# Kernel tuning notes

Hardware: AMD Instinct MI355X
Metric: run time of the kernel (lower is better)

Reference implementation:

```python
import jax, jax.numpy as jnp
import numpy as np

N_NODES, N_EDGES = 50000, 25000
MAX_ARITY, MAX_DEG = 6, 8
NFEAT, NHID, NEMB, NHEADS = 128, 64, 128, 4
BATCH = 4096
ALPHA = 0.2
NEG = -1e9


def _attn_layer(hn_in, he_in, edge_list, node_list, Wn, We, a1, a2, concat):
    # hn_in [N,fin_n], he_in [E,fin_e]; edge_list [E,A] 1-based (0=pad); node_list [N,D] 1-based (0=pad)
    hn = hn_in @ Wn                      # [N,d]
    he = he_in @ We                      # [E,d]
    # --- stage 1: node -> edge attention ---
    emask = edge_list > 0                # [E,A]
    eidx = jnp.where(emask, edge_list - 1, 0)
    nd = hn[eidx]                        # [E,A,d]
    he_b = jnp.broadcast_to(he[:, None, :], nd.shape)
    s1 = jax.nn.leaky_relu(jnp.concatenate([he_b, nd], -1) @ a1, ALPHA)  # [E,A]
    att1 = jax.nn.softmax(jnp.where(emask, s1, NEG), axis=-1)
    edge_out = jnp.einsum('ea,ead->ed', att1, nd)  # [E,d]
    # --- stage 2: edge -> node attention ---
    nmask = node_list > 0                # [N,D]
    nidx = jnp.where(nmask, node_list - 1, 0)
    ed = edge_out[nidx]                  # [N,D,d]
    hn_b = jnp.broadcast_to(hn[:, None, :], ed.shape)
    s2 = jax.nn.leaky_relu(jnp.concatenate([hn_b, ed], -1) @ a2, ALPHA)  # [N,D]
    att2 = jax.nn.softmax(jnp.where(nmask, s2, NEG), axis=-1)
    node_out = jnp.einsum('nd,nde->ne', att2, ed)  # [N,d]
    if concat:
        node_out, edge_out = jax.nn.elu(node_out), jax.nn.elu(edge_out)
    return node_out, edge_out


def _forward(batch_inputs, edge_list, node_list, node_embs, edge_embs,
             Wn, We, a1, a2, Wn_o, We_o, a1_o, a2_o):
    # multi-head layers (vmap over head-stacked params)
    heads = jax.vmap(_attn_layer, in_axes=(None, None, None, None, 0, 0, 0, 0, None))
    hn, he = heads(node_embs, edge_embs, edge_list, node_list, Wn, We, a1, a2, True)
    H, N, d = hn.shape
    out_n = jnp.transpose(hn, (1, 0, 2)).reshape(N, H * d)          # concat heads
    out_e = jnp.transpose(he, (1, 0, 2)).reshape(he.shape[1], H * d)
    # dropout is identity in eval mode
    out_n, out_e = _attn_layer(out_n, out_e, edge_list, node_list, Wn_o, We_o, a1_o, a2_o, False)
    out_n, out_e = jax.nn.elu(out_n), jax.nn.elu(out_e)
    # --- build batch_outputs ---
    B, A1 = batch_inputs.shape
    nemb = out_e.shape[1]
    row0 = out_e[batch_inputs[:, 0] - 1]                            # [B,nemb] (col0 always >0)
    nids = batch_inputs[:, 1:] - 1
    nids = jnp.where(nids < 0, nids + out_n.shape[0], nids)         # torch-style negative wrap
    gathered = out_n[nids]                                          # [B,A1-1,nemb]
    last_nz = jnp.max(jnp.where(batch_inputs != 0, jnp.arange(A1)[None, :], -1), axis=1)  # right-1
    fill = (jnp.arange(1, A1)[None, :] <= last_nz[:, None])[:, :, None]
    rest = jnp.where(fill, gathered, jnp.ones((), gathered.dtype))
    return jnp.concatenate([row0[:, None, :], rest], axis=1)        # [B,A1,nemb]


def setup_inputs() -> dict:
    key = jax.random.key(0)
    ks = jax.random.split(key, 12)
    f32 = jnp.float32
    node_embs = jax.random.normal(ks[0], (N_NODES, NFEAT), f32) * 0.02
    edge_embs = jax.random.normal(ks[1], (N_EDGES, NFEAT), f32) * 0.02
    # ragged incidence with 0-padding (1-based ids)
    el = jax.random.randint(ks[2], (N_EDGES, MAX_ARITY), 1, N_NODES + 1)
    earity = jax.random.randint(ks[3], (N_EDGES, 1), 2, MAX_ARITY + 1)
    edge_list = jnp.where(jnp.arange(MAX_ARITY)[None, :] < earity, el, 0)
    nl = jax.random.randint(ks[4], (N_NODES, MAX_DEG), 1, N_EDGES + 1)
    ndeg = jax.random.randint(ks[5], (N_NODES, 1), 1, MAX_DEG + 1)
    node_list = jnp.where(jnp.arange(MAX_DEG)[None, :] < ndeg, nl, 0)
    # batch: col0 = edge id, cols 1.. = node ids, right-padded with 0
    bi_e = jax.random.randint(ks[6], (BATCH, 1), 1, N_EDGES + 1)
    bi_n = jax.random.randint(ks[7], (BATCH, MAX_ARITY), 1, N_NODES + 1)
    barity = jax.random.randint(ks[8], (BATCH, 1), 2, MAX_ARITY + 1)
    bi_n = jnp.where(jnp.arange(MAX_ARITY)[None, :] < barity, bi_n, 0)
    batch_inputs = jnp.concatenate([bi_e, bi_n], axis=1)
    def glorot(k, shape):
        lim = np.sqrt(6.0 / (shape[-2] + shape[-1]))
        return jax.random.uniform(k, shape, f32, -lim, lim)
    return {
        'batch_inputs': batch_inputs, 'edge_list': edge_list, 'node_list': node_list,
        'node_embs': node_embs, 'edge_embs': edge_embs,
        'Wn': glorot(ks[9], (NHEADS, NFEAT, NHID)),
        'We': glorot(ks[10], (NHEADS, NFEAT, NHID)),
        'a1': jax.random.normal(ks[11], (NHEADS, 2 * NHID), f32) * 0.1,
        'a2': jax.random.normal(jax.random.fold_in(key, 20), (NHEADS, 2 * NHID), f32) * 0.1,
        'Wn_o': glorot(jax.random.fold_in(key, 21), (NHID * NHEADS, NEMB)),
        'We_o': glorot(jax.random.fold_in(key, 22), (NHID * NHEADS, NEMB)),
        'a1_o': jax.random.normal(jax.random.fold_in(key, 23), (2 * NEMB,), f32) * 0.1,
        'a2_o': jax.random.normal(jax.random.fold_in(key, 24), (2 * NEMB,), f32) * 0.1,
    }


def reference(batch_inputs, edge_list, node_list, node_embs, edge_embs,
              Wn, We, a1, a2, Wn_o, We_o, a1_o, a2_o):
    return _forward(batch_inputs, edge_list, node_list, node_embs, edge_embs,
                    Wn, We, a1, a2, Wn_o, We_o, a1_o, a2_o)
```

## Files before the change

### kernel.cpp

```cpp
#include <hip/hip_runtime.h>
#include <math.h>

#define N_NODES 50000
#define N_EDGES 25000
#define MAX_ARITY 6
#define MAX_DEG 8
#define NFEAT 128
#define NHID 64
#define NEMB 128
#define NHEADS 4
#define BATCH 4096

#define MT_N 3128

typedef __bf16 bf16x8 __attribute__((ext_vector_type(8)));
typedef __bf16 bf16x4 __attribute__((ext_vector_type(4)));
typedef float f32x4 __attribute__((ext_vector_type(4)));
typedef float f32x2 __attribute__((ext_vector_type(2)));

__device__ __forceinline__ float wave_sum(float v) {
#pragma unroll
    for (int off = 1; off < 64; off <<= 1) v += __shfl_xor(v, off);
    return v;
}
__device__ __forceinline__ float group32_sum(float v) {
#pragma unroll
    for (int off = 1; off < 32; off <<= 1) v += __shfl_xor(v, off);
    return v;
}
__device__ __forceinline__ float group16_sum(float v) {
#pragma unroll
    for (int off = 1; off < 16; off <<= 1) v += __shfl_xor(v, off);
    return v;
}
__device__ __forceinline__ float group8_sum(float v) {
#pragma unroll
    for (int off = 1; off < 8; off <<= 1) v += __shfl_xor(v, off);
    return v;
}
__device__ __forceinline__ float lrelu(float x) { return x >= 0.f ? x : 0.2f * x; }
__device__ __forceinline__ float eluf(float x) { return x > 0.f ? x : expm1f(x); }

__device__ __forceinline__ int2 pack_fp8x8(const float* v) {
    int w0 = __builtin_amdgcn_cvt_pk_fp8_f32(v[0], v[1], 0, 0);
    w0 = __builtin_amdgcn_cvt_pk_fp8_f32(v[2], v[3], w0, 1);
    int w1 = __builtin_amdgcn_cvt_pk_fp8_f32(v[4], v[5], 0, 0);
    w1 = __builtin_amdgcn_cvt_pk_fp8_f32(v[6], v[7], w1, 1);
    int2 o;
    o.x = w0;
    o.y = w1;
    return o;
}
__device__ __forceinline__ void unpack_fp8x8(int2 w, float* v) {
    f32x2 a = __builtin_amdgcn_cvt_pk_f32_fp8(w.x, false);
    f32x2 b = __builtin_amdgcn_cvt_pk_f32_fp8(w.x, true);
    f32x2 c = __builtin_amdgcn_cvt_pk_f32_fp8(w.y, false);
    f32x2 d = __builtin_amdgcn_cvt_pk_f32_fp8(w.y, true);
    v[0] = a[0]; v[1] = a[1]; v[2] = b[0]; v[3] = b[1];
    v[4] = c[0]; v[5] = c[1]; v[6] = d[0]; v[7] = d[1];
}
__device__ __forceinline__ unsigned char fp8_of(float x) {
    return (unsigned char)(__builtin_amdgcn_cvt_pk_fp8_f32(x, x, 0, 0) & 0xff);
}

#define PREP_BCONV1_BLKS 16
#define PREP_BCONV2_BLKS 16
#define PREP_WVEC1_BLKS 2
#define PREP_WVEC2_BLKS 1
#define PREP_C1_BLKS 6250
#define PREP_TOTAL_BLKS (PREP_BCONV1_BLKS + PREP_BCONV2_BLKS + \
                         PREP_WVEC1_BLKS + PREP_WVEC2_BLKS + PREP_C1_BLKS)

__global__ __launch_bounds__(256) void prep_kernel(
    const float* __restrict__ edge_embs, const float* __restrict__ Wn,
    const float* __restrict__ We, const float* __restrict__ a1, const float* __restrict__ Wn_o,
    const float* __restrict__ We_o, const float* __restrict__ a1_o, __bf16* __restrict__ B1n,
    __bf16* __restrict__ B2n, float* __restrict__ wc1, float* __restrict__ wc2,
    float* __restrict__ c1) {
    int blk = blockIdx.x;
    if (blk < PREP_BCONV1_BLKS) {
        int t = blk * 256 + threadIdx.x;
        int lane = t & 63;
        int nt = (t >> 6) & 15;
        int kt = t >> 10;
        int k0 = kt * 32 + (lane >> 4) * 8;
        int h = nt >> 2;
        int nl = (nt & 3) * 16 + (lane & 15);
        bf16x8 o;
#pragma unroll
        for (int j = 0; j < 8; ++j) o[j] = (__bf16)Wn[(h * NFEAT + k0 + j) * NHID + nl];
        reinterpret_cast<bf16x8*>(B1n)[t] = o;
        return;
    }
    blk -= PREP_BCONV1_BLKS;
    if (blk < PREP_BCONV2_BLKS) {
        int t = blk * 256 + threadIdx.x;
        int lane = t & 63;
        int nt = (t >> 6) & 7;
        int kt = t >> 9;
        int k0 = kt * 32 + (lane >> 4) * 8;
        int n = nt * 16 + (lane & 15);
        bf16x8 o;
#pragma unroll
        for (int j = 0; j < 8; ++j) o[j] = (__bf16)Wn_o[(size_t)(k0 + j) * 128 + n];
        reinterpret_cast<bf16x8*>(B2n)[t] = o;
        return;
    }
    blk -= PREP_BCONV2_BLKS;
    if (blk < PREP_WVEC1_BLKS) {
        int t = blk * 256 + threadIdx.x;
        int h = t >> 7, k = t & 127;
        float s = 0.f;
        for (int j = 0; j < 64; ++j) s += We[(h * NFEAT + k) * NHID + j] * a1[h * 128 + j];
        wc1[t] = s;
        return;
    }
    blk -= PREP_WVEC1_BLKS;
    if (blk < PREP_WVEC2_BLKS) {
        int t = threadIdx.x;
        float s = 0.f;
        for (int j = 0; j < 128; ++j) s += We_o[(size_t)t * 128 + j] * a1_o[j];
        wc2[t] = s;
        return;
    }
    blk -= PREP_WVEC2_BLKS;
    {
        int r = blk * 4 + (threadIdx.x >> 6);
        int lane = threadIdx.x & 63;
        if (r >= N_EDGES) return;
        float x0 = edge_embs[(size_t)r * 128 + lane];
        float x1 = edge_embs[(size_t)r * 128 + 64 + lane];
#pragma unroll
        for (int h = 0; h < 4; ++h) {
            float s = wave_sum(x0 * wc1[h * 128 + lane] + x1 * wc1[h * 128 + 64 + lane]);
            if (lane == 0) c1[r * 4 + h] = s;
        }
    }
}

__global__ __launch_bounds__(256) void mgemm1_kernel(
    const float* __restrict__ Af32, const __bf16* __restrict__ B,
    unsigned char* __restrict__ C, const float* __restrict__ a1v,
    const float* __restrict__ a2v, float* __restrict__ d1, float* __restrict__ g1v) {
    const int w = threadIdx.x >> 6, l = threadIdx.x & 63;
    const int mtb = blockIdx.y * 8 + w * 2;
    const int nbf = blockIdx.x * 4;
    const int lr = l & 15, lk = (l >> 4) * 8;
    f32x4 acc[2][4];
#pragma unroll
    for (int i = 0; i < 2; ++i)
#pragma unroll
        for (int j = 0; j < 4; ++j) acc[i][j] = (f32x4){0.f, 0.f, 0.f, 0.f};
    const bf16x8* Bp = reinterpret_cast<const bf16x8*>(B) + l;
#pragma unroll
    for (int kt = 0; kt < 4; ++kt) {
        bf16x8 a[2];
#pragma unroll
        for (int mi = 0; mi < 2; ++mi) {
            int row = (mtb + mi) * 16 + lr;
            int ks = kt * 32 + lk;
            float v[8];
            if (row < N_NODES) {
                float4 p0 = *reinterpret_cast<const float4*>(Af32 + (size_t)row * 128 + ks);
                float4 p1 = *reinterpret_cast<const float4*>(Af32 + (size_t)row * 128 + ks + 4);
                v[0] = p0.x; v[1] = p0.y; v[2] = p0.z; v[3] = p0.w;
                v[4] = p1.x; v[5] = p1.y; v[6] = p1.z; v[7] = p1.w;
            } else {
#pragma unroll
                for (int j = 0; j < 8; ++j) v[j] = 0.f;
            }
#pragma unroll
            for (int j = 0; j < 8; ++j) a[mi][j] = (__bf16)v[j];
        }
#pragma unroll
        for (int nj = 0; nj < 4; ++nj) {
            bf16x8 b = Bp[((size_t)kt * 16 + nbf + nj) * 64];
#pragma unroll
            for (int mi = 0; mi < 2; ++mi)
                acc[mi][nj] = __builtin_amdgcn_mfma_f32_16x16x32_bf16(a[mi], b, acc[mi][nj], 0, 0, 0);
        }
    }
    const int rq = (l >> 4) * 4;
    const int cl = l & 15;
    const int h = nbf >> 2;
    float va[4], vb[4];
#pragma unroll
    for (int nj = 0; nj < 4; ++nj) {
        int col = ((nbf + nj) & 3) * 16 + cl;
        va[nj] = a1v[h * 128 + 64 + col];
        vb[nj] = a2v[h * 128 + col];
    }
#pragma unroll
    for (int mi = 0; mi < 2; ++mi) {
#pragma unroll
        for (int q = 0; q < 4; ++q) {
            int m = (mtb + mi) * 16 + rq + q;
            float pA = 0.f, pB = 0.f;
#pragma unroll
            for (int nj = 0; nj < 4; ++nj) {
                pA += acc[mi][nj][q] * va[nj];
                pB += acc[mi][nj][q] * vb[nj];
            }
            if (m < N_NODES) {
#pragma unroll
                for (int nj = 0; nj < 4; ++nj)
                    C[(size_t)m * 256 + (nbf + nj) * 16 + cl] = fp8_of(acc[mi][nj][q]);
            }
            pA = group16_sum(pA);
            pB = group16_sum(pB);
            if (cl == 0 && m < N_NODES) {
                d1[m * 4 + h] = pA;
                g1v[m * 4 + h] = pB;
            }
        }
    }
}

__global__ __launch_bounds__(256) void attn64e_kernel(
    const int* __restrict__ nbr, const unsigned char* __restrict__ feat,
    const float* __restrict__ sdot, const float* __restrict__ ndot,
    const float* __restrict__ a2v, const float* __restrict__ wc2,
    unsigned char* __restrict__ eo1, float* __restrict__ f1, float* __restrict__ c2, int rows) {
    const int lane = threadIdx.x & 63;
    const int half = lane >> 5, lp = lane & 31;
    const int r = (blockIdx.x * 4 + (threadIdx.x >> 6)) * 2 + half;
    if (r >= rows) return;
    const int h = lp >> 3;
    int id[MAX_ARITY];
    bool val[MAX_ARITY];
#pragma unroll
    for (int a = 0; a < MAX_ARITY; ++a) {
        int v = nbr[r * MAX_ARITY + a];
        val[a] = v > 0;
        id[a] = val[a] ? (v - 1) : 0;
    }
    int2 f8[MAX_ARITY];
    float nd[MAX_ARITY];
#pragma unroll
    for (int a = 0; a < MAX_ARITY; ++a) {
        f8[a] = *reinterpret_cast<const int2*>(feat + (size_t)id[a] * 256 + lp * 8);
        nd[a] = ndot[(size_t)id[a] * 4 + h];
    }
    const float c = sdot[r * 4 + h];
    float wgt[MAX_ARITY];
    float smax = -1e30f;
#pragma unroll
    for (int a = 0; a < MAX_ARITY; ++a) {
        float s = val[a] ? lrelu(c + nd[a]) : -3e30f;
        wgt[a] = s;
        if (val[a]) smax = fmaxf(smax, s);
    }
    float denom = 0.f;
#pragma unroll
    for (int a = 0; a < MAX_ARITY; ++a) {
        float ex = val[a] ? expf(wgt[a] - smax) : 0.f;
        wgt[a] = ex;
        denom += ex;
    }
    float inv = 1.f / denom;
    float acc[8] = {0.f, 0.f, 0.f, 0.f, 0.f, 0.f, 0.f, 0.f};
#pragma unroll
    for (int a = 0; a < MAX_ARITY; ++a) {
        float fv[8];
        unpack_fp8x8(f8[a], fv);
#pragma unroll
        for (int j = 0; j < 8; ++j) acc[j] = fmaf(wgt[a], fv[j], acc[j]);
    }
#pragma unroll
    for (int j = 0; j < 8; ++j) acc[j] *= inv;
    *reinterpret_cast<int2*>(eo1 + (size_t)r * 256 + lp * 8) = pack_fp8x8(acc);
    float p = 0.f;
#pragma unroll
    for (int j = 0; j < 8; ++j) p += acc[j] * a2v[h * 128 + 64 + (lp & 7) * 8 + j];
    p = group8_sum(p);
    if ((lp & 7) == 0) f1[r * 4 + h] = p;
    float p2 = 0.f;
#pragma unroll
    for (int j = 0; j < 8; ++j) p2 += eluf(acc[j]) * wc2[lp * 8 + j];
    p2 = group32_sum(p2);
    if (lp == 0) c2[r] = p2;
}

#define LDSW 260

__global__ __launch_bounds__(256) void fuse2_kernel(
    const int* __restrict__ nbr, const unsigned char* __restrict__ feat,
    const float* __restrict__ sdot, const float* __restrict__ ndot,
    const __bf16* __restrict__ B, __bf16* __restrict__ hn2, const float* __restrict__ a1o,
    const float* __restrict__ a2o, float* __restrict__ d2, float* __restrict__ g2v) {
    __shared__ __bf16 Alds[64 * LDSW];
    const int w = threadIdx.x >> 6, lane = threadIdx.x & 63;
    const int half = lane >> 5, lp = lane & 31;
    const int h = lp >> 3;
#pragma unroll
    for (int p = 0; p < 8; ++p) {
        const int rl = w * 16 + p * 2 + half;
        const int r = blockIdx.x * 64 + rl;
        __bf16* dptr = &Alds[rl * LDSW + lp * 8];
        if (r >= N_NODES) {
            bf16x8 z;
#pragma unroll
            for (int j = 0; j < 8; ++j) z[j] = (__bf16)0.f;
            *reinterpret_cast<bf16x8*>(dptr) = z;
            continue;
        }
        int id[MAX_DEG];
        bool val[MAX_DEG];
#pragma unroll
        for (int a = 0; a < MAX_DEG; ++a) {
            int v = nbr[r * MAX_DEG + a];
            val[a] = v > 0;
            id[a] = val[a] ? (v - 1) : 0;
        }
        int2 f8[MAX_DEG];
        float nd[MAX_DEG];
#pragma unroll
        for (int a = 0; a < MAX_DEG; ++a) {
            f8[a] = *reinterpret_cast<const int2*>(feat + (size_t)id[a] * 256 + lp * 8);
            nd[a] = ndot[(size_t)id[a] * 4 + h];
        }
        const float c = sdot[r * 4 + h];
        float wgt[MAX_DEG];
        float smax = -1e30f;
#pragma unroll
        for (int a = 0; a < MAX_DEG; ++a) {
            float s = val[a] ? lrelu(c + nd[a]) : -3e30f;
            wgt[a] = s;
            if (val[a]) smax = fmaxf(smax, s);
        }
        float denom = 0.f;
#pragma unroll
        for (int a = 0; a < MAX_DEG; ++a) {
            float ex = val[a] ? expf(wgt[a] - smax) : 0.f;
            wgt[a] = ex;
            denom += ex;
        }
        float inv = 1.f / denom;
        float acc[8] = {0.f, 0.f, 0.f, 0.f, 0.f, 0.f, 0.f, 0.f};
#pragma unroll
        for (int a = 0; a < MAX_DEG; ++a) {
            float fv[8];
            unpack_fp8x8(f8[a], fv);
#pragma unroll
            for (int j = 0; j < 8; ++j) acc[j] = fmaf(wgt[a], fv[j], acc[j]);
        }
        bf16x8 o;
#pragma unroll
        for (int j = 0; j < 8; ++j) o[j] = (__bf16)eluf(acc[j] * inv);
        *reinterpret_cast<bf16x8*>(dptr) = o;
    }
    __syncthreads();
    const int lr = lane & 15, lkq = lane >> 4;
    f32x4 acc[8];
#pragma unroll
    for (int j = 0; j < 8; ++j) acc[j] = (f32x4){0.f, 0.f, 0.f, 0.f};
    const bf16x8* Bp = reinterpret_cast<const bf16x8*>(B) + lane;
#pragma unroll
    for (int kt = 0; kt < 8; ++kt) {
        bf16x8 a = *reinterpret_cast<const bf16x8*>(
            &Alds[(w * 16 + lr) * LDSW + kt * 32 + lkq * 8]);
#pragma unroll
        for (int nj = 0; nj < 8; ++nj) {
            bf16x8 b = Bp[((size_t)kt * 8 + nj) * 64];
            acc[nj] = __builtin_amdgcn_mfma_f32_16x16x32_bf16(a, b, acc[nj], 0, 0, 0);
        }
    }
    const int rq = lkq * 4;
    const int cl = lane & 15;
    const int gm0 = blockIdx.x * 64 + w * 16 + rq;
    float va[8], vb[8];
#pragma unroll
    for (int nj = 0; nj < 8; ++nj) {
        va[nj] = a1o[128 + nj * 16 + cl];
        vb[nj] = a2o[nj * 16 + cl];
    }
#pragma unroll
    for (int q = 0; q < 4; ++q) {
        int m = gm0 + q;
        float pA = 0.f, pB = 0.f;
#pragma unroll
        for (int nj = 0; nj < 8; ++nj) {
            pA += acc[nj][q] * va[nj];
            pB += acc[nj][q] * vb[nj];
        }
        if (m < N_NODES) {
#pragma unroll
            for (int nj = 0; nj < 8; ++nj)
                hn2[(size_t)m * 128 + nj * 16 + cl] = (__bf16)acc[nj][q];
        }
        pA = group16_sum(pA);
        pB = group16_sum(pB);
        if (cl == 0 && m < N_NODES) {
            d2[m] = pA;
            g2v[m] = pB;
        }
    }
}

template <int NNBR, bool DOT>
__global__ __launch_bounds__(256) void attn128_kernel(const int* __restrict__ nbr,
                                                      const __bf16* __restrict__ feat,
                                                      const float* __restrict__ sdot,
                                                      const float* __restrict__ ndot,
                                                      const float* __restrict__ fvec,
                                                      __bf16* __restrict__ outF,
                                                      float* __restrict__ outDot, int rows) {
    const int lane = threadIdx.x & 63;
    const int qt = lane >> 4, lq = lane & 15;
    const int r = (blockIdx.x * 4 + (threadIdx.x >> 6)) * 4 + qt;
    if (r >= rows) return;
    int id[NNBR];
    bool val[NNBR];
#pragma unroll
    for (int a = 0; a < NNBR; ++a) {
        int v = nbr[r * NNBR + a];
        val[a] = v > 0;
        id[a] = val[a] ? (v - 1) : 0;
    }
    bf16x8 f8[NNBR];
    float nd[NNBR];
#pragma unroll
    for (int a = 0; a < NNBR; ++a) {
        f8[a] = *reinterpret_cast<const bf16x8*>(feat + (size_t)id[a] * 128 + lq * 8);
        nd[a] = ndot[id[a]];
    }
    const float c = sdot[r];
    float wgt[NNBR];
    float smax = -1e30f;
#pragma unroll
    for (int a = 0; a < NNBR; ++a) {
        float s = val[a] ? lrelu(c + nd[a]) : -3e30f;
        wgt[a] = s;
        if (val[a]) smax = fmaxf(smax, s);
    }
    float denom = 0.f;
#pragma unroll
    for (int a = 0; a < NNBR; ++a) {
        float ex = val[a] ? expf(wgt[a] - smax) : 0.f;
        wgt[a] = ex;
        denom += ex;
    }
    float inv = 1.f / denom;
    float acc[8] = {0.f, 0.f, 0.f, 0.f, 0.f, 0.f, 0.f, 0.f};
#pragma unroll
    for (int a = 0; a < NNBR; ++a)
#pragma unroll
        for (int j = 0; j < 8; ++j) acc[j] = fmaf(wgt[a], (float)f8[a][j], acc[j]);
    bf16x8 o;
#pragma unroll
    for (int j = 0; j < 8; ++j) {
        acc[j] *= inv;
        o[j] = (__bf16)acc[j];
    }
    *reinterpret_cast<bf16x8*>(outF + (size_t)r * 128 + lq * 8) = o;
    if (DOT) {
        float p = 0.f;
#pragma unroll
        for (int j = 0; j < 8; ++j) p += acc[j] * fvec[128 + lq * 8 + j];
        p = group16_sum(p);
        if (lq == 0) outDot[r] = p;
    }
}

__global__ __launch_bounds__(256) void batch_kernel(const int* __restrict__ bi,
                                                    const __bf16* __restrict__ eo2,
                                                    const __bf16* __restrict__ no2,
                                                    float* __restrict__ out) {
    const int lane = threadIdx.x & 63;
    const int half = lane >> 5, lp = lane & 31;
    const int gw = (blockIdx.x * 4 + (threadIdx.x >> 6)) * 2 + half;
    if (gw >= BATCH * 7) return;
    int b = gw / 7, s = gw % 7;
    int last_nz = -1;
#pragma unroll
    for (int j = 0; j < 7; ++j)
        if (bi[b * 7 + j] != 0) last_nz = j;
    float4 v;
    if (s == 0) {
        int e = bi[b * 7] - 1;
        bf16x4 t = *reinterpret_cast<const bf16x4*>(eo2 + (size_t)e * 128 + lp * 4);
        v = make_float4(eluf((float)t[0]), eluf((float)t[1]), eluf((float)t[2]),
                        eluf((float)t[3]));
    } else if (s <= last_nz) {
        int nid = bi[b * 7 + s] - 1;
        if (nid < 0) nid += N_NODES;
        bf16x4 t = *reinterpret_cast<const bf16x4*>(no2 + (size_t)nid * 128 + lp * 4);
        v = make_float4(eluf((float)t[0]), eluf((float)t[1]), eluf((float)t[2]),
                        eluf((float)t[3]));
    } else {
        v = make_float4(1.f, 1.f, 1.f, 1.f);
    }
    *reinterpret_cast<float4*>(out + (size_t)b * 896 + s * 128 + lp * 4) = v;
}

extern "C" void kernel_launch(void* const* d_in, const int* in_sizes, int n_in,
                              void* d_out, int out_size, void* d_ws, size_t ws_size,
                              hipStream_t stream) {
    const int* batch_inputs = (const int*)d_in[0];
    const int* edge_list = (const int*)d_in[1];
    const int* node_list = (const int*)d_in[2];
    const float* node_embs = (const float*)d_in[3];
    const float* edge_embs = (const float*)d_in[4];
    const float* Wn = (const float*)d_in[5];
    const float* We = (const float*)d_in[6];
    const float* a1 = (const float*)d_in[7];
    const float* a2 = (const float*)d_in[8];
    const float* Wn_o = (const float*)d_in[9];
    const float* We_o = (const float*)d_in[10];
    const float* a1_o = (const float*)d_in[11];
    const float* a2_o = (const float*)d_in[12];
    float* out = (float*)d_out;
    char* ws = (char*)d_ws;

    __bf16* B1n = (__bf16*)(ws);
    __bf16* B2n = (__bf16*)(ws + 65536);
    float* wc1 = (float*)(ws + 131072);
    float* wc2 = (float*)(ws + 133120);
    float* c1 = (float*)(ws + 134144);
    float* d1 = (float*)(ws + 534144);
    float* g1v = (float*)(ws + 1334144);
    float* f1 = (float*)(ws + 2134144);
    float* c2 = (float*)(ws + 2534144);
    float* d2 = (float*)(ws + 2634144);
    float* g2v = (float*)(ws + 2834144);
    float* f2 = (float*)(ws + 3034144);
    unsigned char* hn1 = (unsigned char*)(ws + 3134144);
    __bf16* hn2 = (__bf16*)(ws + 15934144);
    unsigned char* eo1 = (unsigned char*)(ws + 28734144);
    __bf16* eo2 = (__bf16*)(ws + 35134144);
    __bf16* no2 = (__bf16*)(ws + 41534144);

    prep_kernel<<<PREP_TOTAL_BLKS, 256, 0, stream>>>(edge_embs, Wn, We, a1, Wn_o, We_o, a1_o,
                                                     B1n, B2n, wc1, wc2, c1);

    {
        dim3 g(4, MT_N / 8);
        mgemm1_kernel<<<g, 256, 0, stream>>>(node_embs, B1n, hn1, a1, a2, d1, g1v);
    }
    attn64e_kernel<<<(N_EDGES / 2 + 3) / 4, 256, 0, stream>>>(edge_list, hn1, c1, d1, a2, wc2,
                                                              eo1, f1, c2, N_EDGES);
    fuse2_kernel<<<MT_N / 4, 256, 0, stream>>>(node_list, eo1, g1v, f1, B2n, hn2, a1_o, a2_o,
                                               d2, g2v);
    attn128_kernel<MAX_ARITY, true><<<(N_EDGES / 4 + 3) / 4, 256, 0, stream>>>(
        edge_list, hn2, c2, d2, a2_o, eo2, f2, N_EDGES);
    attn128_kernel<MAX_DEG, false><<<(N_NODES / 4 + 3) / 4, 256, 0, stream>>>(
        node_list, eo2, g2v, f2, nullptr, no2, nullptr, N_NODES);
    batch_kernel<<<(BATCH * 7 / 2 + 3) / 4, 256, 0, stream>>>(batch_inputs, eo2, no2, out);
}
```

Baseline: 218.5 us.

## Compute final node attention only for batch-referenced nodes; unfuse layer-2 GEMM

```diff
diff --git a/kernel.cpp b/kernel.cpp
--- a/kernel.cpp
+++ b/kernel.cpp
@@ -216,6 +216,57 @@
     }
 }
 
+__global__ __launch_bounds__(256) void mgemm2_kernel(
+    const __bf16* __restrict__ A, const __bf16* __restrict__ B, __bf16* __restrict__ C,
+    const float* __restrict__ a1o, const float* __restrict__ a2o, float* __restrict__ d2,
+    float* __restrict__ g2v) {
+    const int w = threadIdx.x >> 6, l = threadIdx.x & 63;
+    const int mtb = blockIdx.y * 4 + w;
+    f32x4 acc[8];
+#pragma unroll
+    for (int j = 0; j < 8; ++j) acc[j] = (f32x4){0.f, 0.f, 0.f, 0.f};
+    const bf16x8* Ap = reinterpret_cast<const bf16x8*>(A) + (size_t)mtb * 8 * 64 + l;
+    const bf16x8* Bp = reinterpret_cast<const bf16x8*>(B) + l;
+#pragma unroll
+    for (int kt = 0; kt < 8; ++kt) {
+        bf16x8 a = Ap[(size_t)kt * 64];
+#pragma unroll
+        for (int nj = 0; nj < 8; ++nj) {
+            bf16x8 b = Bp[((size_t)kt * 8 + nj) * 64];
+            acc[nj] = __builtin_amdgcn_mfma_f32_16x16x32_bf16(a, b, acc[nj], 0, 0, 0);
+        }
+    }
+    const int rq = (l >> 4) * 4;
+    const int cl = l & 15;
+    float va[8], vb[8];
+#pragma unroll
+    for (int nj = 0; nj < 8; ++nj) {
+        va[nj] = a1o[128 + nj * 16 + cl];
+        vb[nj] = a2o[nj * 16 + cl];
+    }
+#pragma unroll
+    for (int q = 0; q < 4; ++q) {
+        int m = mtb * 16 + rq + q;
+        float pA = 0.f, pB = 0.f;
+#pragma unroll
+        for (int nj = 0; nj < 8; ++nj) {
+            pA += acc[nj][q] * va[nj];
+            pB += acc[nj][q] * vb[nj];
+        }
+        if (m < N_NODES) {
+#pragma unroll
+            for (int nj = 0; nj < 8; ++nj)
+                C[(size_t)m * 128 + nj * 16 + cl] = (__bf16)acc[nj][q];
+        }
+        pA = group16_sum(pA);
+        pB = group16_sum(pB);
+        if (cl == 0 && m < N_NODES) {
+            d2[m] = pA;
+            g2v[m] = pB;
+        }
+    }
+}
+
 __global__ __launch_bounds__(256) void attn64e_kernel(
     const int* __restrict__ nbr, const unsigned char* __restrict__ feat,
     const float* __restrict__ sdot, const float* __restrict__ ndot,
@@ -281,161 +332,109 @@
     if (lp == 0) c2[r] = p2;
 }
 
-#define LDSW 260
-
-__global__ __launch_bounds__(256) void fuse2_kernel(
-    const int* __restrict__ nbr, const unsigned char* __restrict__ feat,
-    const float* __restrict__ sdot, const float* __restrict__ ndot,
-    const __bf16* __restrict__ B, __bf16* __restrict__ hn2, const float* __restrict__ a1o,
-    const float* __restrict__ a2o, float* __restrict__ d2, float* __restrict__ g2v) {
-    __shared__ __bf16 Alds[64 * LDSW];
-    const int w = threadIdx.x >> 6, lane = threadIdx.x & 63;
-    const int half = lane >> 5, lp = lane & 31;
-    const int h = lp >> 3;
-#pragma unroll
-    for (int p = 0; p < 8; ++p) {
-        const int rl = w * 16 + p * 2 + half;
-        const int r = blockIdx.x * 64 + rl;
-        __bf16* dptr = &Alds[rl * LDSW + lp * 8];
-        if (r >= N_NODES) {
-            bf16x8 z;
-#pragma unroll
-            for (int j = 0; j < 8; ++j) z[j] = (__bf16)0.f;
-            *reinterpret_cast<bf16x8*>(dptr) = z;
-            continue;
-        }
-        int id[MAX_DEG];
-        bool val[MAX_DEG];
-#pragma unroll
-        for (int a = 0; a < MAX_DEG; ++a) {
-            int v = nbr[r * MAX_DEG + a];
-            val[a] = v > 0;
-            id[a] = val[a] ? (v - 1) : 0;
-        }
-        int2 f8[MAX_DEG];
-        float nd[MAX_DEG];
-#pragma unroll
-        for (int a = 0; a < MAX_DEG; ++a) {
-            f8[a] = *reinterpret_cast<const int2*>(feat + (size_t)id[a] * 256 + lp * 8);
-            nd[a] = ndot[(size_t)id[a] * 4 + h];
-        }
-        const float c = sdot[r * 4 + h];
-        float wgt[MAX_DEG];
-        float smax = -1e30f;
-#pragma unroll
-        for (int a = 0; a < MAX_DEG; ++a) {
-            float s = val[a] ? lrelu(c + nd[a]) : -3e30f;
-            wgt[a] = s;
-            if (val[a]) smax = fmaxf(smax, s);
-        }
-        float denom = 0.f;
-#pragma unroll
-        for (int a = 0; a < MAX_DEG; ++a) {
-            float ex = val[a] ? expf(wgt[a] - smax) : 0.f;
-            wgt[a] = ex;
-            denom += ex;
-        }
-        float inv = 1.f / denom;
-        float acc[8] = {0.f, 0.f, 0.f, 0.f, 0.f, 0.f, 0.f, 0.f};
-#pragma unroll
-        for (int a = 0; a < MAX_DEG; ++a) {
-            float fv[8];
-            unpack_fp8x8(f8[a], fv);
-#pragma unroll
-            for (int j = 0; j < 8; ++j) acc[j] = fmaf(wgt[a], fv[j], acc[j]);
-        }
-        bf16x8 o;
-#pragma unroll
-        for (int j = 0; j < 8; ++j) o[j] = (__bf16)eluf(acc[j] * inv);
-        *reinterpret_cast<bf16x8*>(dptr) = o;
-    }
-    __syncthreads();
-    const int lr = lane & 15, lkq = lane >> 4;
-    f32x4 acc[8];
-#pragma unroll
-    for (int j = 0; j < 8; ++j) acc[j] = (f32x4){0.f, 0.f, 0.f, 0.f};
-    const bf16x8* Bp = reinterpret_cast<const bf16x8*>(B) + lane;
-#pragma unroll
-    for (int kt = 0; kt < 8; ++kt) {
-        bf16x8 a = *reinterpret_cast<const bf16x8*>(
-            &Alds[(w * 16 + lr) * LDSW + kt * 32 + lkq * 8]);
-#pragma unroll
-        for (int nj = 0; nj < 8; ++nj) {
-            bf16x8 b = Bp[((size_t)kt * 8 + nj) * 64];
-            acc[nj] = __builtin_amdgcn_mfma_f32_16x16x32_bf16(a, b, acc[nj], 0, 0, 0);
-        }
-    }
-    const int rq = lkq * 4;
-    const int cl = lane & 15;
-    const int gm0 = blockIdx.x * 64 + w * 16 + rq;
-    float va[8], vb[8];
-#pragma unroll
-    for (int nj = 0; nj < 8; ++nj) {
-        va[nj] = a1o[128 + nj * 16 + cl];
-        vb[nj] = a2o[nj * 16 + cl];
-    }
-#pragma unroll
-    for (int q = 0; q < 4; ++q) {
-        int m = gm0 + q;
-        float pA = 0.f, pB = 0.f;
-#pragma unroll
-        for (int nj = 0; nj < 8; ++nj) {
-            pA += acc[nj][q] * va[nj];
-            pB += acc[nj][q] * vb[nj];
-        }
-        if (m < N_NODES) {
-#pragma unroll
-            for (int nj = 0; nj < 8; ++nj)
-                hn2[(size_t)m * 128 + nj * 16 + cl] = (__bf16)acc[nj][q];
-        }
-        pA = group16_sum(pA);
-        pB = group16_sum(pB);
-        if (cl == 0 && m < N_NODES) {
-            d2[m] = pA;
-            g2v[m] = pB;
-        }
-    }
-}
-
-template <int NNBR, bool DOT>
-__global__ __launch_bounds__(256) void attn128_kernel(const int* __restrict__ nbr,
-                                                      const __bf16* __restrict__ feat,
+__global__ __launch_bounds__(256) void attn64n_kernel(const int* __restrict__ nbr,
+                                                      const unsigned char* __restrict__ feat,
                                                       const float* __restrict__ sdot,
                                                       const float* __restrict__ ndot,
-                                                      const float* __restrict__ fvec,
-                                                      __bf16* __restrict__ outF,
-                                                      float* __restrict__ outDot, int rows) {
+                                                      __bf16* __restrict__ Afrag, int rows,
+                                                      int rowsPad) {
+    const int lane = threadIdx.x & 63;
+    const int half = lane >> 5, lp = lane & 31;
+    const int r = (blockIdx.x * 4 + (threadIdx.x >> 6)) * 2 + half;
+    if (r >= rowsPad) return;
+    const int rr = r & 15, mt = r >> 4;
+    const int kt = lp >> 2, g = lp & 3;
+    __bf16* dptr = Afrag + ((((size_t)mt * 8 + kt) * 64 + g * 16 + rr) << 3);
+    if (r >= rows) {
+        bf16x8 z;
+#pragma unroll
+        for (int j = 0; j < 8; ++j) z[j] = (__bf16)0.f;
+        *reinterpret_cast<bf16x8*>(dptr) = z;
+        return;
+    }
+    const int h = lp >> 3;
+    int id[MAX_DEG];
+    bool val[MAX_DEG];
+#pragma unroll
+    for (int a = 0; a < MAX_DEG; ++a) {
+        int v = nbr[r * MAX_DEG + a];
+        val[a] = v > 0;
+        id[a] = val[a] ? (v - 1) : 0;
+    }
+    int2 f8[MAX_DEG];
+    float nd[MAX_DEG];
+#pragma unroll
+    for (int a = 0; a < MAX_DEG; ++a) {
+        f8[a] = *reinterpret_cast<const int2*>(feat + (size_t)id[a] * 256 + lp * 8);
+        nd[a] = ndot[(size_t)id[a] * 4 + h];
+    }
+    const float c = sdot[r * 4 + h];
+    float wgt[MAX_DEG];
+    float smax = -1e30f;
+#pragma unroll
+    for (int a = 0; a < MAX_DEG; ++a) {
+        float s = val[a] ? lrelu(c + nd[a]) : -3e30f;
+        wgt[a] = s;
+        if (val[a]) smax = fmaxf(smax, s);
+    }
+    float denom = 0.f;
+#pragma unroll
+    for (int a = 0; a < MAX_DEG; ++a) {
+        float ex = val[a] ? expf(wgt[a] - smax) : 0.f;
+        wgt[a] = ex;
+        denom += ex;
+    }
+    float inv = 1.f / denom;
+    float acc[8] = {0.f, 0.f, 0.f, 0.f, 0.f, 0.f, 0.f, 0.f};
+#pragma unroll
+    for (int a = 0; a < MAX_DEG; ++a) {
+        float fv[8];
+        unpack_fp8x8(f8[a], fv);
+#pragma unroll
+        for (int j = 0; j < 8; ++j) acc[j] = fmaf(wgt[a], fv[j], acc[j]);
+    }
+    bf16x8 o;
+#pragma unroll
+    for (int j = 0; j < 8; ++j) o[j] = (__bf16)eluf(acc[j] * inv);
+    *reinterpret_cast<bf16x8*>(dptr) = o;
+}
+
+__global__ __launch_bounds__(256) void attn128e_kernel(
+    const int* __restrict__ nbr, const __bf16* __restrict__ feat,
+    const float* __restrict__ sdot, const float* __restrict__ ndot,
+    const float* __restrict__ fvec, __bf16* __restrict__ outF, float* __restrict__ outDot,
+    int rows) {
     const int lane = threadIdx.x & 63;
     const int qt = lane >> 4, lq = lane & 15;
     const int r = (blockIdx.x * 4 + (threadIdx.x >> 6)) * 4 + qt;
     if (r >= rows) return;
-    int id[NNBR];
-    bool val[NNBR];
-#pragma unroll
-    for (int a = 0; a < NNBR; ++a) {
-        int v = nbr[r * NNBR + a];
+    int id[MAX_ARITY];
+    bool val[MAX_ARITY];
+#pragma unroll
+    for (int a = 0; a < MAX_ARITY; ++a) {
+        int v = nbr[r * MAX_ARITY + a];
         val[a] = v > 0;
         id[a] = val[a] ? (v - 1) : 0;
     }
-    bf16x8 f8[NNBR];
-    float nd[NNBR];
-#pragma unroll
-    for (int a = 0; a < NNBR; ++a) {
+    bf16x8 f8[MAX_ARITY];
+    float nd[MAX_ARITY];
+#pragma unroll
+    for (int a = 0; a < MAX_ARITY; ++a) {
         f8[a] = *reinterpret_cast<const bf16x8*>(feat + (size_t)id[a] * 128 + lq * 8);
         nd[a] = ndot[id[a]];
     }
     const float c = sdot[r];
-    float wgt[NNBR];
+    float wgt[MAX_ARITY];
     float smax = -1e30f;
 #pragma unroll
-    for (int a = 0; a < NNBR; ++a) {
+    for (int a = 0; a < MAX_ARITY; ++a) {
         float s = val[a] ? lrelu(c + nd[a]) : -3e30f;
         wgt[a] = s;
         if (val[a]) smax = fmaxf(smax, s);
     }
     float denom = 0.f;
 #pragma unroll
-    for (int a = 0; a < NNBR; ++a) {
+    for (int a = 0; a < MAX_ARITY; ++a) {
         float ex = val[a] ? expf(wgt[a] - smax) : 0.f;
         wgt[a] = ex;
         denom += ex;
@@ -443,7 +442,7 @@
     float inv = 1.f / denom;
     float acc[8] = {0.f, 0.f, 0.f, 0.f, 0.f, 0.f, 0.f, 0.f};
 #pragma unroll
-    for (int a = 0; a < NNBR; ++a)
+    for (int a = 0; a < MAX_ARITY; ++a)
 #pragma unroll
         for (int j = 0; j < 8; ++j) acc[j] = fmaf(wgt[a], (float)f8[a][j], acc[j]);
     bf16x8 o;
@@ -453,24 +452,22 @@
         o[j] = (__bf16)acc[j];
     }
     *reinterpret_cast<bf16x8*>(outF + (size_t)r * 128 + lq * 8) = o;
-    if (DOT) {
-        float p = 0.f;
-#pragma unroll
-        for (int j = 0; j < 8; ++j) p += acc[j] * fvec[128 + lq * 8 + j];
-        p = group16_sum(p);
-        if (lq == 0) outDot[r] = p;
-    }
-}
-
-__global__ __launch_bounds__(256) void batch_kernel(const int* __restrict__ bi,
-                                                    const __bf16* __restrict__ eo2,
-                                                    const __bf16* __restrict__ no2,
-                                                    float* __restrict__ out) {
+    float p = 0.f;
+#pragma unroll
+    for (int j = 0; j < 8; ++j) p += acc[j] * fvec[128 + lq * 8 + j];
+    p = group16_sum(p);
+    if (lq == 0) outDot[r] = p;
+}
+
+__global__ __launch_bounds__(256) void batch2_kernel(
+    const int* __restrict__ bi, const int* __restrict__ node_list,
+    const __bf16* __restrict__ eo2, const float* __restrict__ g2v,
+    const float* __restrict__ f2, float* __restrict__ out) {
     const int lane = threadIdx.x & 63;
     const int half = lane >> 5, lp = lane & 31;
     const int gw = (blockIdx.x * 4 + (threadIdx.x >> 6)) * 2 + half;
     if (gw >= BATCH * 7) return;
-    int b = gw / 7, s = gw % 7;
+    const int b = gw / 7, s = gw % 7;
     int last_nz = -1;
 #pragma unroll
     for (int j = 0; j < 7; ++j)
@@ -483,10 +480,45 @@
                         eluf((float)t[3]));
     } else if (s <= last_nz) {
         int nid = bi[b * 7 + s] - 1;
-        if (nid < 0) nid += N_NODES;
-        bf16x4 t = *reinterpret_cast<const bf16x4*>(no2 + (size_t)nid * 128 + lp * 4);
-        v = make_float4(eluf((float)t[0]), eluf((float)t[1]), eluf((float)t[2]),
-                        eluf((float)t[3]));
+        int id[MAX_DEG];
+        bool val[MAX_DEG];
+#pragma unroll
+        for (int a = 0; a < MAX_DEG; ++a) {
+            int e = node_list[nid * MAX_DEG + a];
+            val[a] = e > 0;
+            id[a] = val[a] ? (e - 1) : 0;
+        }
+        bf16x4 f8[MAX_DEG];
+        float nd[MAX_DEG];
+#pragma unroll
+        for (int a = 0; a < MAX_DEG; ++a) {
+            f8[a] = *reinterpret_cast<const bf16x4*>(eo2 + (size_t)id[a] * 128 + lp * 4);
+            nd[a] = f2[id[a]];
+        }
+        const float c = g2v[nid];
+        float wgt[MAX_DEG];
+        float smax = -1e30f;
+#pragma unroll
+        for (int a = 0; a < MAX_DEG; ++a) {
+            float sc = val[a] ? lrelu(c + nd[a]) : -3e30f;
+            wgt[a] = sc;
+            if (val[a]) smax = fmaxf(smax, sc);
+        }
+        float denom = 0.f;
+#pragma unroll
+        for (int a = 0; a < MAX_DEG; ++a) {
+            float ex = val[a] ? expf(wgt[a] - smax) : 0.f;
+            wgt[a] = ex;
+            denom += ex;
+        }
+        float inv = 1.f / denom;
+        float acc[4] = {0.f, 0.f, 0.f, 0.f};
+#pragma unroll
+        for (int a = 0; a < MAX_DEG; ++a)
+#pragma unroll
+            for (int j = 0; j < 4; ++j) acc[j] = fmaf(wgt[a], (float)f8[a][j], acc[j]);
+        v = make_float4(eluf(acc[0] * inv), eluf(acc[1] * inv), eluf(acc[2] * inv),
+                        eluf(acc[3] * inv));
     } else {
         v = make_float4(1.f, 1.f, 1.f, 1.f);
     }
@@ -525,10 +557,10 @@
     float* g2v = (float*)(ws + 2834144);
     float* f2 = (float*)(ws + 3034144);
     unsigned char* hn1 = (unsigned char*)(ws + 3134144);
-    __bf16* hn2 = (__bf16*)(ws + 15934144);
-    unsigned char* eo1 = (unsigned char*)(ws + 28734144);
-    __bf16* eo2 = (__bf16*)(ws + 35134144);
-    __bf16* no2 = (__bf16*)(ws + 41534144);
+    __bf16* A2n = (__bf16*)(ws + 15934144);
+    __bf16* hn2 = (__bf16*)(ws + 41558720);
+    unsigned char* eo1 = (unsigned char*)(ws + 54358720);
+    __bf16* eo2 = (__bf16*)(ws + 60758720);
 
     prep_kernel<<<PREP_TOTAL_BLKS, 256, 0, stream>>>(edge_embs, Wn, We, a1, Wn_o, We_o, a1_o,
                                                      B1n, B2n, wc1, wc2, c1);
@@ -539,11 +571,14 @@
     }
     attn64e_kernel<<<(N_EDGES / 2 + 3) / 4, 256, 0, stream>>>(edge_list, hn1, c1, d1, a2, wc2,
                                                               eo1, f1, c2, N_EDGES);
-    fuse2_kernel<<<MT_N / 4, 256, 0, stream>>>(node_list, eo1, g1v, f1, B2n, hn2, a1_o, a2_o,
-                                               d2, g2v);
-    attn128_kernel<MAX_ARITY, true><<<(N_EDGES / 4 + 3) / 4, 256, 0, stream>>>(
-        edge_list, hn2, c2, d2, a2_o, eo2, f2, N_EDGES);
-    attn128_kernel<MAX_DEG, false><<<(N_NODES / 4 + 3) / 4, 256, 0, stream>>>(
-        node_list, eo2, g2v, f2, nullptr, no2, nullptr, N_NODES);
-    batch_kernel<<<(BATCH * 7 / 2 + 3) / 4, 256, 0, stream>>>(batch_inputs, eo2, no2, out);
-}
+    attn64n_kernel<<<(MT_N * 16 / 2 + 3) / 4, 256, 0, stream>>>(node_list, eo1, g1v, f1, A2n,
+                                                                N_NODES, MT_N * 16);
+    {
+        dim3 g(1, MT_N / 4);
+        mgemm2_kernel<<<g, 256, 0, stream>>>(A2n, B2n, hn2, a1_o, a2_o, d2, g2v);
+    }
+    attn128e_kernel<<<(N_EDGES / 4 + 3) / 4, 256, 0, stream>>>(edge_list, hn2, c2, d2, a2_o,
+                                                               eo2, f2, N_EDGES);
+    batch2_kernel<<<(BATCH * 7 / 2 + 3) / 4, 256, 0, stream>>>(batch_inputs, node_list, eo2,
+                                                               g2v, f2, out);
+}
```

New measurement: 209.1 us. 4.3% less time.
